# Kernel optimization log

Hardware: AMD Instinct MI355X
Metric: run time of the kernel (lower is better)

## Reference

```python
import jax, jax.numpy as jnp
import numpy as np

VOCAB, D, A, NEG = 32000, 200, 20, 2
NUM_USERS, NUM_ITEMS = 100000, 50000
R, L, B, NNZ = 4096, 128, 1024, 20480
EPS = 1e-12

def _norm(x, axis):
    n = jnp.sqrt(jnp.sum(x * x, axis=axis, keepdims=True))
    return x / jnp.maximum(n, EPS)

def setup_inputs() -> dict:
    key = jax.random.key(0)
    ks = jax.random.split(key, 20)
    rows_u = jax.random.randint(ks[5], (NNZ,), 0, B)
    cols_u = jax.random.randint(ks[6], (NNZ,), 0, R)
    rows_i = jax.random.randint(ks[7], (NNZ,), 0, B)
    cols_i = jax.random.randint(ks[8], (NNZ,), 0, R)
    return {
        "historical_review": jax.random.randint(ks[0], (R, L), 0, VOCAB),
        "neg_review": jax.random.randint(ks[1], (R * NEG, L), 0, VOCAB),
        "user": jax.random.randint(ks[2], (B,), 0, NUM_USERS),
        "item": jax.random.randint(ks[3], (B,), 0, NUM_ITEMS),
        "label": jax.random.uniform(ks[4], (B,), jnp.float32, 1.0, 5.0),
        "user_histor_index": jnp.stack([rows_u, cols_u]),
        "user_histor_value": jax.random.uniform(ks[9], (NNZ,), jnp.float32),
        "item_histor_index": jnp.stack([rows_i, cols_i]),
        "item_histor_value": jax.random.uniform(ks[10], (NNZ,), jnp.float32),
        "word_emb": jax.random.normal(ks[11], (VOCAB, D), jnp.float32),
        "Wm": jax.random.normal(ks[12], (D, D), jnp.float32) * 0.05,
        "Ww": jax.random.normal(ks[13], (A, D), jnp.float32) * 0.05,
        "bw": jnp.zeros((A,), jnp.float32),
        "Wt": jax.random.normal(ks[14], (D, A), jnp.float32) * 0.05,
        "fc_w": jax.random.uniform(ks[15], (1, 2 * D), jnp.float32, -0.05, 0.05),
        "fc_b": jnp.zeros((1,), jnp.float32),
        "fm_V": jax.random.uniform(ks[16], (2 * D, 10), jnp.float32, -0.05, 0.05),
        "b_users": jax.random.uniform(ks[17], (NUM_USERS, 1), jnp.float32, 0.0, 0.1),
        "b_items": jax.random.uniform(ks[18], (NUM_ITEMS, 1), jnp.float32, 0.0, 0.1),
    }

def reference(historical_review, neg_review, user, item, label,
              user_histor_index, user_histor_value,
              item_histor_index, item_histor_value,
              word_emb, Wm, Ww, bw, Wt, fc_w, fc_b, fm_V, b_users, b_items):
    # ABAE attention over each review
    e_w = word_emb[historical_review]              # (R, L, D)
    y_s = jnp.mean(e_w, axis=1)                    # (R, D)
    z_n = jnp.mean(word_emb[neg_review], axis=1)   # (R*NEG, D)
    dx = jnp.einsum('rld,rd->rl', e_w @ Wm.T, y_s) # (R, L)
    ax = jax.nn.softmax(dx, axis=1)
    # Faithful to source: view(R, D, L) is a raw reshape, not a transpose.
    z_s = jnp.einsum('rdl,rl->rd', e_w.reshape(R, D, L), ax)  # (R, D)
    p_t = z_s @ Ww.T + bw                          # (R, A)
    r_s = p_t @ Wt.T                               # (R, D)
    # cosine margin ranking loss
    c1 = jnp.sum(_norm(r_s, 1) * _norm(z_s, 1), axis=-1)      # (R,)
    c1 = jnp.repeat(c1, NEG)                                   # (R*NEG,)
    c2 = jnp.sum(_norm(z_n.reshape(R, NEG, D), 2) * _norm(r_s, 1)[:, None, :], axis=-1).reshape(-1)
    abae_out_loss = jax.nn.relu(c2 - c1 + 1.0)     # margin=1, target=+1
    J_loss = jnp.mean(abae_out_loss)
    # aspect-matrix orthogonality regularizer
    Tn = _norm(Wt, 0)                              # normalize columns (dim=0)
    U_loss = jnp.mean((Tn.T @ Tn - jnp.eye(A, dtype=Wt.dtype)) ** 2)
    # sparse (B, R) @ (R, D) aggregation via segment_sum
    user_aspect_embed = jax.ops.segment_sum(
        user_histor_value[:, None] * r_s[user_histor_index[1]],
        user_histor_index[0], num_segments=B)      # (B, D)
    item_aspect_embed = jax.ops.segment_sum(
        item_histor_value[:, None] * r_s[item_histor_index[1]],
        item_histor_index[0], num_segments=B)      # (B, D)
    input_vec = jnp.concatenate([user_aspect_embed, item_aspect_embed], axis=1)  # (B, 2D)
    fm_linear = input_vec @ fc_w.T + fc_b          # (B, 1)
    fm_i1 = (input_vec @ fm_V) ** 2
    fm_i2 = (input_vec ** 2) @ (fm_V ** 2)
    # NOTE: faithful to source, the quadratic term is summed over the whole batch (scalar)
    fm_output = 0.5 * jnp.sum(fm_i1 - fm_i2) + fm_linear + b_users[user] + b_items[item]
    prediction = fm_output.squeeze(1)              # (B,)
    rating_loss = (prediction - label) ** 2
    mse_loss = jnp.mean(rating_loss)
    obj_loss = mse_loss + 0.01 * J_loss + 0.01 * U_loss
    return (obj_loss, rating_loss, abae_out_loss, prediction, user_aspect_embed, item_aspect_embed)
```

## Files before the change

kernel.cpp:

```cpp
#include <hip/hip_runtime.h>
#include <hip/hip_fp16.h>
#include <math.h>

#define R_TOT 4096
#define L_LEN 128
#define D_DIM 200
#define A_DIM 20
#define NEGK  2
#define B_SZ  1024
#define NNZ_C 20480
#define RN_TOT (R_TOT*NEGK)
#define S_TOT (R_TOT + RN_TOT)
#define VOCAB_C 32000
#define EPS_ 1e-12f
#define SLOT_CAP 64
#define NBUCK_BLK 160

__device__ __forceinline__ float4 unpack4(const uint2 u) {
  union { unsigned v; __half2 h; } c0, c1;
  c0.v = u.x; c1.v = u.y;
  const float2 f0 = __half22float2(c0.h);
  const float2 f1 = __half22float2(c1.h);
  return make_float4(f0.x, f0.y, f1.x, f1.y);
}

__device__ __forceinline__ float dot8h(const uint4 q, const float4 va, const float4 vb) {
  const float4 e0 = unpack4(make_uint2(q.x, q.y));
  const float4 e1 = unpack4(make_uint2(q.z, q.w));
  return e0.x*va.x + e0.y*va.y + e0.z*va.z + e0.w*va.w
       + e1.x*vb.x + e1.y*vb.y + e1.z*vb.z + e1.w*vb.w;
}

#define DPPI(old_, src_, ctrl, rmask) \
  __builtin_amdgcn_update_dpp(old_, src_, ctrl, rmask, 0xf, false)

__device__ __forceinline__ float dpp_sum32(float s) {
  s += __int_as_float(DPPI(0, __float_as_int(s), 0x111, 0xf));
  s += __int_as_float(DPPI(0, __float_as_int(s), 0x112, 0xf));
  s += __int_as_float(DPPI(0, __float_as_int(s), 0x114, 0xf));
  s += __int_as_float(DPPI(0, __float_as_int(s), 0x118, 0xf));
  s += __int_as_float(DPPI(0, __float_as_int(s), 0x142, 0xa));
  return s;
}
__device__ __forceinline__ float dpp_sum64(float s) {
  s = dpp_sum32(s);
  s += __int_as_float(DPPI(0, __float_as_int(s), 0x143, 0xc));
  return s;
}
__device__ __forceinline__ float dpp_max64(float s) {
  s = fmaxf(s, __int_as_float(DPPI(__float_as_int(s), __float_as_int(s), 0x111, 0xf)));
  s = fmaxf(s, __int_as_float(DPPI(__float_as_int(s), __float_as_int(s), 0x112, 0xf)));
  s = fmaxf(s, __int_as_float(DPPI(__float_as_int(s), __float_as_int(s), 0x114, 0xf)));
  s = fmaxf(s, __int_as_float(DPPI(__float_as_int(s), __float_as_int(s), 0x118, 0xf)));
  s = fmaxf(s, __int_as_float(DPPI(__float_as_int(s), __float_as_int(s), 0x142, 0xa)));
  s = fmaxf(s, __int_as_float(DPPI(__float_as_int(s), __float_as_int(s), 0x143, 0xc)));
  return s;
}

__global__ __launch_bounds__(256) void k_cast(
    const float* __restrict__ emb, ushort* __restrict__ emb_h, int* __restrict__ cnt)
{
  if (blockIdx.x == 0) {
    for (int i = threadIdx.x; i < 2*B_SZ; i += 256) cnt[i] = 0;
  }
  const int idx = blockIdx.x*256 + threadIdx.x;
  if (idx < (VOCAB_C*D_DIM)/4) {
    const float4 v = reinterpret_cast<const float4*>(emb)[idx];
    ushort4 o;
    o.x = __half_as_ushort(__float2half(v.x));
    o.y = __half_as_ushort(__float2half(v.y));
    o.z = __half_as_ushort(__float2half(v.z));
    o.w = __half_as_ushort(__float2half(v.w));
    reinterpret_cast<ushort4*>(emb_h)[idx] = o;
  }
}

#define ACC8(Q) { \
  const float4 e0_ = unpack4(make_uint2((Q).x,(Q).y)); \
  const float4 e1_ = unpack4(make_uint2((Q).z,(Q).w)); \
  sA.x+=e0_.x; sA.y+=e0_.y; sA.z+=e0_.z; sA.w+=e0_.w; \
  sB.x+=e1_.x; sB.y+=e1_.y; sB.z+=e1_.z; sB.w+=e1_.w; }

__global__ __launch_bounds__(256, 8) void k_means2(
    const int* __restrict__ hist, const int* __restrict__ neg,
    const ushort* __restrict__ emb_h,
    float* __restrict__ ys_all, float* __restrict__ zn_all,
    const int* __restrict__ uidx, const float* __restrict__ uval,
    const int* __restrict__ iidx, const float* __restrict__ ival,
    int* __restrict__ cnt, int* __restrict__ scol, float* __restrict__ sval)
{
  const int sb = blockIdx.x;
  const int tid = threadIdx.x;

  if (sb >= S_TOT) {
    const int g = (sb - S_TOT)*256 + tid;
    if (g < NNZ_C) {
      const int b = uidx[g];
      const int slot = atomicAdd(&cnt[b], 1);
      if (slot < SLOT_CAP) {
        scol[b*SLOT_CAP + slot] = uidx[NNZ_C + g];
        sval[b*SLOT_CAP + slot] = uval[g];
      }
    } else {
      const int g2 = g - NNZ_C;
      const int b = iidx[g2];
      const int slot = atomicAdd(&cnt[B_SZ + b], 1);
      if (slot < SLOT_CAP) {
        scol[(B_SZ + b)*SLOT_CAP + slot] = iidx[NNZ_C + g2];
        sval[(B_SZ + b)*SLOT_CAP + slot] = ival[g2];
      }
    }
    return;
  }

  __shared__ int widx[L_LEN];
  __shared__ __align__(16) float part[8][D_DIM];
  const bool is_pos = (sb < R_TOT);
  const int* src = is_pos ? (hist + (size_t)sb*L_LEN)
                          : (neg + (size_t)(sb - R_TOT)*L_LEN);
  if (tid < L_LEN) widx[tid] = src[tid];
  __syncthreads();

  const int c5 = tid & 31;
  const int j  = tid >> 5;
  float4 sA = {0.f,0.f,0.f,0.f}, sB = {0.f,0.f,0.f,0.f};
  if (c5 < 25) {
    const size_t coff = 8*c5;
    uint4 q0 = *reinterpret_cast<const uint4*>(emb_h + (size_t)widx[j +   0]*D_DIM + coff);
    uint4 q1 = *reinterpret_cast<const uint4*>(emb_h + (size_t)widx[j +   8]*D_DIM + coff);
    uint4 q2 = *reinterpret_cast<const uint4*>(emb_h + (size_t)widx[j +  16]*D_DIM + coff);
    uint4 q3 = *reinterpret_cast<const uint4*>(emb_h + (size_t)widx[j +  24]*D_DIM + coff);
    uint4 q4 = *reinterpret_cast<const uint4*>(emb_h + (size_t)widx[j +  32]*D_DIM + coff);
    uint4 q5 = *reinterpret_cast<const uint4*>(emb_h + (size_t)widx[j +  40]*D_DIM + coff);
    uint4 q6 = *reinterpret_cast<const uint4*>(emb_h + (size_t)widx[j +  48]*D_DIM + coff);
    uint4 q7 = *reinterpret_cast<const uint4*>(emb_h + (size_t)widx[j +  56]*D_DIM + coff);
    ACC8(q0) ACC8(q1) ACC8(q2) ACC8(q3) ACC8(q4) ACC8(q5) ACC8(q6) ACC8(q7)
    q0 = *reinterpret_cast<const uint4*>(emb_h + (size_t)widx[j +  64]*D_DIM + coff);
    q1 = *reinterpret_cast<const uint4*>(emb_h + (size_t)widx[j +  72]*D_DIM + coff);
    q2 = *reinterpret_cast<const uint4*>(emb_h + (size_t)widx[j +  80]*D_DIM + coff);
    q3 = *reinterpret_cast<const uint4*>(emb_h + (size_t)widx[j +  88]*D_DIM + coff);
    q4 = *reinterpret_cast<const uint4*>(emb_h + (size_t)widx[j +  96]*D_DIM + coff);
    q5 = *reinterpret_cast<const uint4*>(emb_h + (size_t)widx[j + 104]*D_DIM + coff);
    q6 = *reinterpret_cast<const uint4*>(emb_h + (size_t)widx[j + 112]*D_DIM + coff);
    q7 = *reinterpret_cast<const uint4*>(emb_h + (size_t)widx[j + 120]*D_DIM + coff);
    ACC8(q0) ACC8(q1) ACC8(q2) ACC8(q3) ACC8(q4) ACC8(q5) ACC8(q6) ACC8(q7)
    *reinterpret_cast<float4*>(&part[j][8*c5])     = sA;
    *reinterpret_cast<float4*>(&part[j][8*c5 + 4]) = sB;
  }
  __syncthreads();
  float* dst = is_pos ? (ys_all + (size_t)sb*D_DIM)
                      : (zn_all + (size_t)(sb - R_TOT)*D_DIM);
  if (tid < D_DIM) {
    float a = 0.f;
    #pragma unroll
    for (int j2 = 0; j2 < 8; ++j2) a += part[j2][tid];
    dst[tid] = a * (1.0f/128.0f);
  }
}

#define KB_RT 16
__global__ __launch_bounds__(256, 2) void k_matvec(
    const float* __restrict__ ys_all, const float* __restrict__ Wm,
    float* __restrict__ vv_all)
{
  __shared__ float ysl[KB_RT][D_DIM];
  const int r0 = blockIdx.x * KB_RT;
  const int tid = threadIdx.x;
  for (int i = tid; i < KB_RT*D_DIM; i += 256)
    ysl[i / D_DIM][i % D_DIM] = ys_all[(size_t)r0*D_DIM + i];
  __syncthreads();
  if (tid < D_DIM) {
    float acc[KB_RT];
    #pragma unroll
    for (int r = 0; r < KB_RT; ++r) acc[r] = 0.f;
    #pragma unroll 4
    for (int k = 0; k < D_DIM; ++k) {
      const float w = Wm[k*D_DIM + tid];
      #pragma unroll
      for (int r = 0; r < KB_RT; ++r) acc[r] += ysl[r][k] * w;
    }
    #pragma unroll
    for (int r = 0; r < KB_RT; ++r)
      vv_all[(size_t)(r0 + r)*D_DIM + tid] = acc[r];
  }
}

__global__ __launch_bounds__(512, 6) void k_attn(
    const int* __restrict__ hist, const ushort* __restrict__ emb_h,
    const float* __restrict__ vv_all,
    const float* __restrict__ Ww, const float* __restrict__ bw,
    const float* __restrict__ Wt, const float* __restrict__ zn_all,
    float* __restrict__ rs_out, float* __restrict__ abae)
{
  __shared__ __align__(16) float part[D_DIM][16];
  __shared__ __align__(16) float ax[L_LEN];
  __shared__ __align__(16) float zs[D_DIM];
  __shared__ __align__(16) float ubuf[240];
  int*   widx  = reinterpret_cast<int*>(ubuf);
  float* ptile = ubuf;
  float* red   = ubuf + 160;

  const int r = blockIdx.x;
  const int tid = threadIdx.x, lane = tid & 63, wv = tid >> 6;
  const int c5 = tid & 31;
  const int j  = tid >> 5;
  const bool act = (c5 < 25);
  const int coff = 8*c5;

  if (tid < L_LEN) widx[tid] = hist[r*L_LEN + tid];
  float4 v8a = {0,0,0,0}, v8b = {0,0,0,0};
  if (act) {
    v8a = *reinterpret_cast<const float4*>(vv_all + (size_t)r*D_DIM + coff);
    v8b = *reinterpret_cast<const float4*>(vv_all + (size_t)r*D_DIM + coff + 4);
  }
  __syncthreads();

  uint4 q0,q1,q2,q3,q4,q5,q6,q7;
  q0=q1=q2=q3=q4=q5=q6=q7=make_uint4(0,0,0,0);
  float zn0 = 0.f, zn1 = 0.f;
  float p0=0.f,p1=0.f,p2=0.f,p3=0.f,p4=0.f,p5=0.f,p6=0.f,p7=0.f;
  if (act) {
    q0 = *reinterpret_cast<const uint4*>(emb_h + (size_t)widx[j +   0]*D_DIM + coff);
    q1 = *reinterpret_cast<const uint4*>(emb_h + (size_t)widx[j +  16]*D_DIM + coff);
    q2 = *reinterpret_cast<const uint4*>(emb_h + (size_t)widx[j +  32]*D_DIM + coff);
    q3 = *reinterpret_cast<const uint4*>(emb_h + (size_t)widx[j +  48]*D_DIM + coff);
    q4 = *reinterpret_cast<const uint4*>(emb_h + (size_t)widx[j +  64]*D_DIM + coff);
    q5 = *reinterpret_cast<const uint4*>(emb_h + (size_t)widx[j +  80]*D_DIM + coff);
    q6 = *reinterpret_cast<const uint4*>(emb_h + (size_t)widx[j +  96]*D_DIM + coff);
    q7 = *reinterpret_cast<const uint4*>(emb_h + (size_t)widx[j + 112]*D_DIM + coff);
  }
  if (tid < D_DIM) {
    zn0 = zn_all[(size_t)(2*r)*D_DIM + tid];
    zn1 = zn_all[(size_t)(2*r + 1)*D_DIM + tid];
  }
  if (act) {
    p0 = dot8h(q0, v8a, v8b); p1 = dot8h(q1, v8a, v8b);
    p2 = dot8h(q2, v8a, v8b); p3 = dot8h(q3, v8a, v8b);
    p4 = dot8h(q4, v8a, v8b); p5 = dot8h(q5, v8a, v8b);
    p6 = dot8h(q6, v8a, v8b); p7 = dot8h(q7, v8a, v8b);
  }
  p0 = dpp_sum32(p0); p1 = dpp_sum32(p1); p2 = dpp_sum32(p2); p3 = dpp_sum32(p3);
  p4 = dpp_sum32(p4); p5 = dpp_sum32(p5); p6 = dpp_sum32(p6); p7 = dpp_sum32(p7);
  if (c5 == 31) {
    ax[j]      = p0; ax[j + 16]  = p1; ax[j + 32]  = p2; ax[j + 48]  = p3;
    ax[j + 64] = p4; ax[j + 80]  = p5; ax[j + 96]  = p6; ax[j + 112] = p7;
  }
  __syncthreads();

  if (tid < 64) {
    float m = dpp_max64(fmaxf(ax[tid], ax[tid+64]));
    if (tid == 63) red[0] = m;
  }
  __syncthreads();
  const float M = red[0];
  if (tid < L_LEN) {
    const float e = expf(ax[tid] - M);
    ax[tid] = e;
    const float s = dpp_sum64(e);
    if (lane == 63) red[1 + wv] = s;
  }
  __syncthreads();

  if (act) {
    const int Y  = 25*j + c5;
    const int l0 = (8*Y) & 127;
    const int v0 = Y >> 4;
    const int sl = Y & 15;
    const float4 ax8a = *reinterpret_cast<const float4*>(ax + l0);
    const float4 ax8b = *reinterpret_cast<const float4*>(ax + l0 + 4);
    part[v0 +   0][sl] = dot8h(q0, ax8a, ax8b);
    part[v0 +  25][sl] = dot8h(q1, ax8a, ax8b);
    part[v0 +  50][sl] = dot8h(q2, ax8a, ax8b);
    part[v0 +  75][sl] = dot8h(q3, ax8a, ax8b);
    part[v0 + 100][sl] = dot8h(q4, ax8a, ax8b);
    part[v0 + 125][sl] = dot8h(q5, ax8a, ax8b);
    part[v0 + 150][sl] = dot8h(q6, ax8a, ax8b);
    part[v0 + 175][sl] = dot8h(q7, ax8a, ax8b);
  }
  __syncthreads();

  if (tid < D_DIM) {
    const float Sinv = 1.0f / (red[1] + red[2]);
    const float4 a0 = *reinterpret_cast<const float4*>(&part[tid][0]);
    const float4 a1 = *reinterpret_cast<const float4*>(&part[tid][4]);
    const float4 a2 = *reinterpret_cast<const float4*>(&part[tid][8]);
    const float4 a3 = *reinterpret_cast<const float4*>(&part[tid][12]);
    const float s = ((a0.x+a0.y)+(a0.z+a0.w)) + ((a1.x+a1.y)+(a1.z+a1.w))
                  + ((a2.x+a2.y)+(a2.z+a2.w)) + ((a3.x+a3.y)+(a3.z+a3.w));
    zs[tid] = s * Sinv;
  }
  __syncthreads();

  if (tid < 160) {
    const int a = tid % 20, jj = tid / 20;
    float s = 0.f;
    #pragma unroll
    for (int ii = 0; ii < 25; ++ii) {
      const int d = jj + 8*ii;
      s += zs[d] * Ww[a*D_DIM + d];
    }
    ptile[tid] = s;
  }
  __syncthreads();
  if (tid < A_DIM) {
    float s = bw[tid];
    #pragma unroll
    for (int jj = 0; jj < 8; ++jj) s += ptile[jj*20 + tid];
    red[2 + tid] = s;
  }
  __syncthreads();

  float rsd = 0.f, zsd = 0.f;
  if (tid < D_DIM) {
    float acc = 0.f;
    #pragma unroll
    for (int a = 0; a < A_DIM; ++a) acc += red[2+a] * Wt[tid*A_DIM + a];
    rsd = acc; zsd = zs[tid];
    rs_out[(size_t)r*D_DIM + tid] = acc;
  } else { zn0 = 0.f; zn1 = 0.f; }
  float a0 = dpp_sum64(rsd*rsd), a1 = dpp_sum64(zsd*zsd), a2 = dpp_sum64(rsd*zsd);
  float b0 = dpp_sum64(zn0*zn0), b1 = dpp_sum64(zn0*rsd);
  float b2 = dpp_sum64(zn1*zn1), b3 = dpp_sum64(zn1*rsd);
  if (lane == 63) {
    red[22 + 0*8 + wv] = a0; red[22 + 1*8 + wv] = a1; red[22 + 2*8 + wv] = a2;
    red[22 + 3*8 + wv] = b0; red[22 + 4*8 + wv] = b1;
    red[22 + 5*8 + wv] = b2; red[22 + 6*8 + wv] = b3;
  }
  __syncthreads();

  if (tid < 64) {
    const int qi = tid >> 3, k = tid & 7;
    float v = (qi < 7) ? red[22 + 8*qi + k] : 0.f;
    v += __shfl_xor(v, 1); v += __shfl_xor(v, 2); v += __shfl_xor(v, 4);
    const float s0 = __shfl(v, 0),  s1 = __shfl(v, 8),  s2 = __shfl(v, 16);
    const float t0 = __shfl(v, 24), t1 = __shfl(v, 32);
    const float t2 = __shfl(v, 40), t3 = __shfl(v, 48);
    if (tid == 0) {
      const float nr = fmaxf(sqrtf(s0), EPS_);
      const float nz = fmaxf(sqrtf(s1), EPS_);
      const float c1 = s2 / (nr * nz);
      const float c2a = t1 / (fmaxf(sqrtf(t0), EPS_) * nr);
      const float c2b = t3 / (fmaxf(sqrtf(t2), EPS_) * nr);
      abae[2*r]     = fmaxf(c2a - c1 + 1.0f, 0.0f);
      abae[2*r + 1] = fmaxf(c2b - c1 + 1.0f, 0.0f);
    }
  }
}

__global__ __launch_bounds__(512) void k_aggfm(
    const int* __restrict__ cnt, const int* __restrict__ scol,
    const float* __restrict__ sval, const float* __restrict__ rs,
    const float* __restrict__ fcw, const float* __restrict__ V,
    float* __restrict__ uae, float* __restrict__ iae,
    float* __restrict__ linb, float* __restrict__ quadb)
{
  __shared__ __align__(16) float ivec[2*D_DIM];
  __shared__ float redw[8];
  __shared__ float qpart[10];
  const int b = blockIdx.x;
  const int tid = threadIdx.x, lane = tid & 63, wv = tid >> 6;

  if (tid < D_DIM) {
    int n = cnt[b]; n = n < SLOT_CAP ? n : SLOT_CAP;
    const int* cols = scol + (size_t)b*SLOT_CAP;
    const float* vals = sval + (size_t)b*SLOT_CAP;
    float acc = 0.f;
    for (int j = 0; j < n; ++j) acc += vals[j] * rs[(size_t)cols[j]*D_DIM + tid];
    ivec[tid] = acc;
    uae[(size_t)b*D_DIM + tid] = acc;
  } else if (tid >= 256 && tid < 256 + D_DIM) {
    const int t = tid - 256;
    int n = cnt[B_SZ + b]; n = n < SLOT_CAP ? n : SLOT_CAP;
    const int* cols = scol + (size_t)(B_SZ + b)*SLOT_CAP;
    const float* vals = sval + (size_t)(B_SZ + b)*SLOT_CAP;
    float acc = 0.f;
    for (int j = 0; j < n; ++j) acc += vals[j] * rs[(size_t)cols[j]*D_DIM + t];
    ivec[D_DIM + t] = acc;
    iae[(size_t)b*D_DIM + t] = acc;
  }
  __syncthreads();

  float lv = 0.f;
  if (tid < 2*D_DIM) lv = ivec[tid] * fcw[tid];
  #pragma unroll
  for (int o = 32; o > 0; o >>= 1) lv += __shfl_xor(lv, o);
  if (lane == 0) redw[wv] = lv;

  {
    const int k = wv;
    float s1 = 0.f, s2 = 0.f;
    for (int f = lane; f < 2*D_DIM; f += 64) {
      const float x = ivec[f];
      const float vk = V[f*10 + k];
      s1 += x*vk; s2 += x*x*vk*vk;
    }
    #pragma unroll
    for (int o = 32; o > 0; o >>= 1) { s1 += __shfl_xor(s1,o); s2 += __shfl_xor(s2,o); }
    if (lane == 0) qpart[k] = s1*s1 - s2;
  }
  if (wv < 2) {
    const int k = 8 + wv;
    float s1 = 0.f, s2 = 0.f;
    for (int f = lane; f < 2*D_DIM; f += 64) {
      const float x = ivec[f];
      const float vk = V[f*10 + k];
      s1 += x*vk; s2 += x*x*vk*vk;
    }
    #pragma unroll
    for (int o = 32; o > 0; o >>= 1) { s1 += __shfl_xor(s1,o); s2 += __shfl_xor(s2,o); }
    if (lane == 0) qpart[k] = s1*s1 - s2;
  }
  __syncthreads();
  if (tid == 0) {
    float lin = 0.f;
    #pragma unroll
    for (int i = 0; i < 8; ++i) lin += redw[i];
    float q = 0.f;
    #pragma unroll
    for (int i = 0; i < 10; ++i) q += qpart[i];
    linb[b] = lin; quadb[b] = q;
  }
}

__global__ __launch_bounds__(1024) void k_final2(
    const float* __restrict__ quadb, const float* __restrict__ linb,
    const float* __restrict__ fcb, const int* __restrict__ user,
    const int* __restrict__ item, const float* __restrict__ busers,
    const float* __restrict__ bitems, const float* __restrict__ label,
    const float* __restrict__ Wt, const float* __restrict__ abae,
    float* __restrict__ pred, float* __restrict__ rl, float* __restrict__ obj)
{
  __shared__ float sA[16], sB[16], sC[16];
  __shared__ float cninv[A_DIM];
  __shared__ float quad_s;
  const int tid = threadIdx.x;
  const int lane = tid & 63;
  const int wv = tid >> 6;

  float q = quadb[tid];
  #pragma unroll
  for (int o = 32; o > 0; o >>= 1) q += __shfl_xor(q, o);
  if (lane == 0) sA[wv] = q;

  if (tid < A_DIM) {
    float s = 0.f;
    for (int d = 0; d < D_DIM; ++d) { const float w = Wt[d*A_DIM + tid]; s += w*w; }
    cninv[tid] = 1.0f / fmaxf(sqrtf(s), EPS_);
  }
  __syncthreads();
  if (wv == 0) {
    float s = (lane < 16) ? sA[lane] : 0.f;
    #pragma unroll
    for (int o = 32; o > 0; o >>= 1) s += __shfl_xor(s, o);
    if (lane == 0) quad_s = s;
  }
  __syncthreads();

  const float p = 0.5f*quad_s + linb[tid] + fcb[0]
                + busers[user[tid]] + bitems[item[tid]];
  pred[tid] = p;
  const float dd = p - label[tid];
  const float myrl = dd*dd;
  rl[tid] = myrl;

  float u = 0.f;
  if (tid < 400) {
    const int a = tid / 20, c = tid % 20;
    float dot = 0.f;
    for (int d = 0; d < D_DIM; ++d) dot += Wt[d*A_DIM + a]*Wt[d*A_DIM + c];
    const float g = dot*cninv[a]*cninv[c] - (a==c ? 1.0f : 0.0f);
    u = g*g;
  }
  float js = 0.f;
  #pragma unroll
  for (int j = 0; j < 8; ++j) js += abae[tid + 1024*j];
  float ms = myrl;

  #pragma unroll
  for (int o = 32; o > 0; o >>= 1) {
    u += __shfl_xor(u,o); js += __shfl_xor(js,o); ms += __shfl_xor(ms,o);
  }
  if (lane == 0) { sA[wv] = u; sB[wv] = js; sC[wv] = ms; }
  __syncthreads();
  if (tid == 0) {
    float U = 0.f, J = 0.f, Ms = 0.f;
    for (int i = 0; i < 16; ++i) { U += sA[i]; J += sB[i]; Ms += sC[i]; }
    obj[0] = Ms/1024.0f + 0.01f*(J/8192.0f) + 0.01f*(U/400.0f);
  }
}

extern "C" void kernel_launch(void* const* d_in, const int* in_sizes, int n_in,
                              void* d_out, int out_size, void* d_ws, size_t ws_size,
                              hipStream_t stream) {
  const int*   hist   = (const int*)  d_in[0];
  const int*   neg    = (const int*)  d_in[1];
  const int*   user   = (const int*)  d_in[2];
  const int*   item   = (const int*)  d_in[3];
  const float* label  = (const float*)d_in[4];
  const int*   uidx   = (const int*)  d_in[5];
  const float* uval   = (const float*)d_in[6];
  const int*   iidx   = (const int*)  d_in[7];
  const float* ival   = (const float*)d_in[8];
  const float* emb    = (const float*)d_in[9];
  const float* Wm     = (const float*)d_in[10];
  const float* Ww     = (const float*)d_in[11];
  const float* bw     = (const float*)d_in[12];
  const float* Wt     = (const float*)d_in[13];
  const float* fcw    = (const float*)d_in[14];
  const float* fcb    = (const float*)d_in[15];
  const float* V      = (const float*)d_in[16];
  const float* busers = (const float*)d_in[17];
  const float* bitems = (const float*)d_in[18];

  float* out  = (float*)d_out;
  float* obj  = out;
  float* rl   = out + 1;
  float* abae = out + 1 + B_SZ;
  float* pred = out + 1 + B_SZ + RN_TOT;
  float* uae  = pred + B_SZ;
  float* iae  = uae + (size_t)B_SZ*D_DIM;

  float* ws     = (float*)d_ws;
  float* rs     = ws;
  float* ys_all = rs + (size_t)R_TOT*D_DIM;
  float* zn_all = ys_all + (size_t)R_TOT*D_DIM;
  float* vv_all = zn_all + (size_t)RN_TOT*D_DIM;
  float* linb   = vv_all + (size_t)R_TOT*D_DIM;
  float* quadb  = linb + B_SZ;
  float* sval   = quadb + B_SZ;
  int*   scol   = (int*)(sval + (size_t)2*B_SZ*SLOT_CAP);
  int*   cnt    = scol + (size_t)2*B_SZ*SLOT_CAP;
  ushort* emb_h = (ushort*)(cnt + 2*B_SZ);

  const int cast_blocks = (VOCAB_C*D_DIM/4 + 255)/256;

  k_cast  <<<cast_blocks, 256, 0, stream>>>(emb, emb_h, cnt);
  k_means2<<<S_TOT + NBUCK_BLK, 256, 0, stream>>>(hist, neg, emb_h,
                                                  ys_all, zn_all,
                                                  uidx, uval, iidx, ival,
                                                  cnt, scol, sval);
  k_matvec<<<R_TOT/KB_RT, 256, 0, stream>>>(ys_all, Wm, vv_all);
  k_attn  <<<R_TOT, 512, 0, stream>>>(hist, emb_h, vv_all, Ww, bw, Wt,
                                      zn_all, rs, abae);
  k_aggfm <<<B_SZ, 512, 0, stream>>>(cnt, scol, sval, rs, fcw, V,
                                     uae, iae, linb, quadb);
  k_final2<<<1, 1024, 0, stream>>>(quadb, linb, fcb, user, item, busers, bitems,
                                   label, Wt, abae, pred, rl, obj);
}
```

Baseline: 297.1 us.

## Split embedding mean gather into two vocab-half passes and move U/J loss reductions into aggfm

The mean-embedding gather now runs as two launches, each handling only words in one half of the vocabulary (masked loads redirected to row 0). The aim is to keep each pass's half-table in the L2/MALL cache. The second pass adds its partial sum to the first and finalizes the mean. Separately, the Wt orthogonality loss and the abae sum move out of the single-block final kernel into two extra blocks of k_aggfm. In exchange the gather issues twice as many loads, the output is read back once, and there is one extra launch.

New measurement: 279.9 us. 5.8% less time.

```diff
diff --git a/kernel.cpp b/kernel.cpp
--- a/kernel.cpp
+++ b/kernel.cpp
@@ -12,6 +12,7 @@
 #define RN_TOT (R_TOT*NEGK)
 #define S_TOT (R_TOT + RN_TOT)
 #define VOCAB_C 32000
+#define VHALF 16000
 #define EPS_ 1e-12f
 #define SLOT_CAP 64
 #define NBUCK_BLK 160
@@ -75,19 +76,22 @@
   }
 }
 
-#define ACC8(Q) { \
+#define ACC8M(Q, M) { \
   const float4 e0_ = unpack4(make_uint2((Q).x,(Q).y)); \
   const float4 e1_ = unpack4(make_uint2((Q).z,(Q).w)); \
-  sA.x+=e0_.x; sA.y+=e0_.y; sA.z+=e0_.z; sA.w+=e0_.w; \
-  sB.x+=e1_.x; sB.y+=e1_.y; sB.z+=e1_.z; sB.w+=e1_.w; }
-
-__global__ __launch_bounds__(256, 8) void k_means2(
+  sA.x = fmaf(M, e0_.x, sA.x); sA.y = fmaf(M, e0_.y, sA.y); \
+  sA.z = fmaf(M, e0_.z, sA.z); sA.w = fmaf(M, e0_.w, sA.w); \
+  sB.x = fmaf(M, e1_.x, sB.x); sB.y = fmaf(M, e1_.y, sB.y); \
+  sB.z = fmaf(M, e1_.z, sB.z); sB.w = fmaf(M, e1_.w, sB.w); }
+
+__global__ __launch_bounds__(256, 8) void k_means_phase(
     const int* __restrict__ hist, const int* __restrict__ neg,
     const ushort* __restrict__ emb_h,
     float* __restrict__ ys_all, float* __restrict__ zn_all,
     const int* __restrict__ uidx, const float* __restrict__ uval,
     const int* __restrict__ iidx, const float* __restrict__ ival,
-    int* __restrict__ cnt, int* __restrict__ scol, float* __restrict__ sval)
+    int* __restrict__ cnt, int* __restrict__ scol, float* __restrict__ sval,
+    int lo, int finalize)
 {
   const int sb = blockIdx.x;
   const int tid = threadIdx.x;
@@ -126,24 +130,28 @@
   float4 sA = {0.f,0.f,0.f,0.f}, sB = {0.f,0.f,0.f,0.f};
   if (c5 < 25) {
     const size_t coff = 8*c5;
-    uint4 q0 = *reinterpret_cast<const uint4*>(emb_h + (size_t)widx[j +   0]*D_DIM + coff);
-    uint4 q1 = *reinterpret_cast<const uint4*>(emb_h + (size_t)widx[j +   8]*D_DIM + coff);
-    uint4 q2 = *reinterpret_cast<const uint4*>(emb_h + (size_t)widx[j +  16]*D_DIM + coff);
-    uint4 q3 = *reinterpret_cast<const uint4*>(emb_h + (size_t)widx[j +  24]*D_DIM + coff);
-    uint4 q4 = *reinterpret_cast<const uint4*>(emb_h + (size_t)widx[j +  32]*D_DIM + coff);
-    uint4 q5 = *reinterpret_cast<const uint4*>(emb_h + (size_t)widx[j +  40]*D_DIM + coff);
-    uint4 q6 = *reinterpret_cast<const uint4*>(emb_h + (size_t)widx[j +  48]*D_DIM + coff);
-    uint4 q7 = *reinterpret_cast<const uint4*>(emb_h + (size_t)widx[j +  56]*D_DIM + coff);
-    ACC8(q0) ACC8(q1) ACC8(q2) ACC8(q3) ACC8(q4) ACC8(q5) ACC8(q6) ACC8(q7)
-    q0 = *reinterpret_cast<const uint4*>(emb_h + (size_t)widx[j +  64]*D_DIM + coff);
-    q1 = *reinterpret_cast<const uint4*>(emb_h + (size_t)widx[j +  72]*D_DIM + coff);
-    q2 = *reinterpret_cast<const uint4*>(emb_h + (size_t)widx[j +  80]*D_DIM + coff);
-    q3 = *reinterpret_cast<const uint4*>(emb_h + (size_t)widx[j +  88]*D_DIM + coff);
-    q4 = *reinterpret_cast<const uint4*>(emb_h + (size_t)widx[j +  96]*D_DIM + coff);
-    q5 = *reinterpret_cast<const uint4*>(emb_h + (size_t)widx[j + 104]*D_DIM + coff);
-    q6 = *reinterpret_cast<const uint4*>(emb_h + (size_t)widx[j + 112]*D_DIM + coff);
-    q7 = *reinterpret_cast<const uint4*>(emb_h + (size_t)widx[j + 120]*D_DIM + coff);
-    ACC8(q0) ACC8(q1) ACC8(q2) ACC8(q3) ACC8(q4) ACC8(q5) ACC8(q6) ACC8(q7)
+    #pragma unroll
+    for (int half = 0; half < 2; ++half) {
+      const int base = j + 64*half;
+      int   wv_[8]; float m_[8];
+      #pragma unroll
+      for (int k = 0; k < 8; ++k) {
+        const int w = widx[base + 8*k];
+        const bool in = ((unsigned)(w - lo) < (unsigned)VHALF);
+        wv_[k] = in ? w : 0;
+        m_[k]  = in ? 1.f : 0.f;
+      }
+      const uint4 q0 = *reinterpret_cast<const uint4*>(emb_h + (size_t)wv_[0]*D_DIM + coff);
+      const uint4 q1 = *reinterpret_cast<const uint4*>(emb_h + (size_t)wv_[1]*D_DIM + coff);
+      const uint4 q2 = *reinterpret_cast<const uint4*>(emb_h + (size_t)wv_[2]*D_DIM + coff);
+      const uint4 q3 = *reinterpret_cast<const uint4*>(emb_h + (size_t)wv_[3]*D_DIM + coff);
+      const uint4 q4 = *reinterpret_cast<const uint4*>(emb_h + (size_t)wv_[4]*D_DIM + coff);
+      const uint4 q5 = *reinterpret_cast<const uint4*>(emb_h + (size_t)wv_[5]*D_DIM + coff);
+      const uint4 q6 = *reinterpret_cast<const uint4*>(emb_h + (size_t)wv_[6]*D_DIM + coff);
+      const uint4 q7 = *reinterpret_cast<const uint4*>(emb_h + (size_t)wv_[7]*D_DIM + coff);
+      ACC8M(q0, m_[0]) ACC8M(q1, m_[1]) ACC8M(q2, m_[2]) ACC8M(q3, m_[3])
+      ACC8M(q4, m_[4]) ACC8M(q5, m_[5]) ACC8M(q6, m_[6]) ACC8M(q7, m_[7])
+    }
     *reinterpret_cast<float4*>(&part[j][8*c5])     = sA;
     *reinterpret_cast<float4*>(&part[j][8*c5 + 4]) = sB;
   }
@@ -154,7 +162,8 @@
     float a = 0.f;
     #pragma unroll
     for (int j2 = 0; j2 < 8; ++j2) a += part[j2][tid];
-    dst[tid] = a * (1.0f/128.0f);
+    if (finalize) dst[tid] = (dst[tid] + a) * (1.0f/128.0f);
+    else          dst[tid] = a;
   }
 }
 
@@ -351,14 +360,62 @@
     const int* __restrict__ cnt, const int* __restrict__ scol,
     const float* __restrict__ sval, const float* __restrict__ rs,
     const float* __restrict__ fcw, const float* __restrict__ V,
+    const float* __restrict__ Wt, const float* __restrict__ abae,
     float* __restrict__ uae, float* __restrict__ iae,
-    float* __restrict__ linb, float* __restrict__ quadb)
+    float* __restrict__ linb, float* __restrict__ quadb,
+    float* __restrict__ uj)
 {
   __shared__ __align__(16) float ivec[2*D_DIM];
   __shared__ float redw[8];
   __shared__ float qpart[10];
+  __shared__ float cninvS[A_DIM];
   const int b = blockIdx.x;
   const int tid = threadIdx.x, lane = tid & 63, wv = tid >> 6;
+
+  if (b == B_SZ) {
+    if (tid < 400) {
+      const int a = tid / 20, c = tid % 20;
+      float dot = 0.f;
+      #pragma unroll 4
+      for (int d = 0; d < D_DIM; ++d) dot += Wt[d*A_DIM + a] * Wt[d*A_DIM + c];
+      ivec[tid] = dot;
+    }
+    __syncthreads();
+    if (tid < A_DIM) cninvS[tid] = 1.0f / fmaxf(sqrtf(ivec[tid*21]), EPS_);
+    __syncthreads();
+    float u = 0.f;
+    if (tid < 400) {
+      const int a = tid / 20, c = tid % 20;
+      const float g = ivec[tid]*cninvS[a]*cninvS[c] - (a==c ? 1.0f : 0.0f);
+      u = g*g;
+    }
+    #pragma unroll
+    for (int o = 32; o > 0; o >>= 1) u += __shfl_xor(u, o);
+    if (lane == 0) redw[wv] = u;
+    __syncthreads();
+    if (tid == 0) {
+      float s = 0.f;
+      #pragma unroll
+      for (int i = 0; i < 8; ++i) s += redw[i];
+      uj[0] = s;
+    }
+    return;
+  }
+  if (b == B_SZ + 1) {
+    float s = 0.f;
+    for (int i = tid; i < RN_TOT; i += 512) s += abae[i];
+    #pragma unroll
+    for (int o = 32; o > 0; o >>= 1) s += __shfl_xor(s, o);
+    if (lane == 0) redw[wv] = s;
+    __syncthreads();
+    if (tid == 0) {
+      float t = 0.f;
+      #pragma unroll
+      for (int i = 0; i < 8; ++i) t += redw[i];
+      uj[1] = t;
+    }
+    return;
+  }
 
   if (tid < D_DIM) {
     int n = cnt[b]; n = n < SLOT_CAP ? n : SLOT_CAP;
@@ -427,11 +484,10 @@
     const float* __restrict__ fcb, const int* __restrict__ user,
     const int* __restrict__ item, const float* __restrict__ busers,
     const float* __restrict__ bitems, const float* __restrict__ label,
-    const float* __restrict__ Wt, const float* __restrict__ abae,
+    const float* __restrict__ uj,
     float* __restrict__ pred, float* __restrict__ rl, float* __restrict__ obj)
 {
-  __shared__ float sA[16], sB[16], sC[16];
-  __shared__ float cninv[A_DIM];
+  __shared__ float sA[16], sC[16];
   __shared__ float quad_s;
   const int tid = threadIdx.x;
   const int lane = tid & 63;
@@ -441,12 +497,6 @@
   #pragma unroll
   for (int o = 32; o > 0; o >>= 1) q += __shfl_xor(q, o);
   if (lane == 0) sA[wv] = q;
-
-  if (tid < A_DIM) {
-    float s = 0.f;
-    for (int d = 0; d < D_DIM; ++d) { const float w = Wt[d*A_DIM + tid]; s += w*w; }
-    cninv[tid] = 1.0f / fmaxf(sqrtf(s), EPS_);
-  }
   __syncthreads();
   if (wv == 0) {
     float s = (lane < 16) ? sA[lane] : 0.f;
@@ -463,29 +513,15 @@
   const float myrl = dd*dd;
   rl[tid] = myrl;
 
-  float u = 0.f;
-  if (tid < 400) {
-    const int a = tid / 20, c = tid % 20;
-    float dot = 0.f;
-    for (int d = 0; d < D_DIM; ++d) dot += Wt[d*A_DIM + a]*Wt[d*A_DIM + c];
-    const float g = dot*cninv[a]*cninv[c] - (a==c ? 1.0f : 0.0f);
-    u = g*g;
-  }
-  float js = 0.f;
+  float ms = myrl;
   #pragma unroll
-  for (int j = 0; j < 8; ++j) js += abae[tid + 1024*j];
-  float ms = myrl;
-
-  #pragma unroll
-  for (int o = 32; o > 0; o >>= 1) {
-    u += __shfl_xor(u,o); js += __shfl_xor(js,o); ms += __shfl_xor(ms,o);
-  }
-  if (lane == 0) { sA[wv] = u; sB[wv] = js; sC[wv] = ms; }
+  for (int o = 32; o > 0; o >>= 1) ms += __shfl_xor(ms, o);
+  if (lane == 0) sC[wv] = ms;
   __syncthreads();
   if (tid == 0) {
-    float U = 0.f, J = 0.f, Ms = 0.f;
-    for (int i = 0; i < 16; ++i) { U += sA[i]; J += sB[i]; Ms += sC[i]; }
-    obj[0] = Ms/1024.0f + 0.01f*(J/8192.0f) + 0.01f*(U/400.0f);
+    float Ms = 0.f;
+    for (int i = 0; i < 16; ++i) Ms += sC[i];
+    obj[0] = Ms/1024.0f + 0.01f*(uj[1]/8192.0f) + 0.01f*(uj[0]/400.0f);
   }
 }
 
@@ -531,19 +567,24 @@
   int*   scol   = (int*)(sval + (size_t)2*B_SZ*SLOT_CAP);
   int*   cnt    = scol + (size_t)2*B_SZ*SLOT_CAP;
   ushort* emb_h = (ushort*)(cnt + 2*B_SZ);
+  float* uj     = vv_all;
 
   const int cast_blocks = (VOCAB_C*D_DIM/4 + 255)/256;
 
-  k_cast  <<<cast_blocks, 256, 0, stream>>>(emb, emb_h, cnt);
-  k_means2<<<S_TOT + NBUCK_BLK, 256, 0, stream>>>(hist, neg, emb_h,
-                                                  ys_all, zn_all,
-                                                  uidx, uval, iidx, ival,
-                                                  cnt, scol, sval);
-  k_matvec<<<R_TOT/KB_RT, 256, 0, stream>>>(ys_all, Wm, vv_all);
-  k_attn  <<<R_TOT, 512, 0, stream>>>(hist, emb_h, vv_all, Ww, bw, Wt,
-                                      zn_all, rs, abae);
-  k_aggfm <<<B_SZ, 512, 0, stream>>>(cnt, scol, sval, rs, fcw, V,
-                                     uae, iae, linb, quadb);
-  k_final2<<<1, 1024, 0, stream>>>(quadb, linb, fcb, user, item, busers, bitems,
-                                   label, Wt, abae, pred, rl, obj);
-}
+  k_cast       <<<cast_blocks, 256, 0, stream>>>(emb, emb_h, cnt);
+  k_means_phase<<<S_TOT + NBUCK_BLK, 256, 0, stream>>>(hist, neg, emb_h,
+                                                       ys_all, zn_all,
+                                                       uidx, uval, iidx, ival,
+                                                       cnt, scol, sval, 0, 0);
+  k_means_phase<<<S_TOT, 256, 0, stream>>>(hist, neg, emb_h,
+                                           ys_all, zn_all,
+                                           uidx, uval, iidx, ival,
+                                           cnt, scol, sval, VHALF, 1);
+  k_matvec     <<<R_TOT/KB_RT, 256, 0, stream>>>(ys_all, Wm, vv_all);
+  k_attn       <<<R_TOT, 512, 0, stream>>>(hist, emb_h, vv_all, Ww, bw, Wt,
+                                           zn_all, rs, abae);
+  k_aggfm      <<<B_SZ + 2, 512, 0, stream>>>(cnt, scol, sval, rs, fcw, V, Wt, abae,
+                                              uae, iae, linb, quadb, uj);
+  k_final2     <<<1, 1024, 0, stream>>>(quadb, linb, fcb, user, item, busers, bitems,
+                                        label, uj, pred, rl, obj);
+}
```
